# Kernel tuning notes

Hardware: AMD Instinct MI355X
Metric: run time of the kernel (lower is better)

## Reference

```python
import jax, jax.numpy as jnp
import numpy as np

N_NODES = 100000
N_EDGES = 1600000
VOCAB = 50000
F_DIM = 128
N_GRAPHS = 64
N_LABELS = 20


def setup_inputs() -> dict:
    key = jax.random.key(0)
    ks = jax.random.split(key, 12)
    s = 1.0 / np.sqrt(F_DIM)
    inp = {
        "x": jax.random.randint(ks[0], (N_NODES,), 0, VOCAB),
        "edge_index": jax.random.randint(ks[1], (2, N_EDGES), 0, N_NODES),
        "batch": jnp.sort(jax.random.randint(ks[2], (N_NODES,), 0, N_GRAPHS)),
        "emb": jax.random.normal(ks[3], (VOCAB, F_DIM), jnp.float32),
        "w1_rel": jax.random.normal(ks[4], (F_DIM, F_DIM), jnp.float32) * s,
        "w1_root": jax.random.normal(ks[5], (F_DIM, F_DIM), jnp.float32) * s,
        "b1": jnp.zeros((F_DIM,), jnp.float32),
        "w2_rel": jax.random.normal(ks[6], (F_DIM, F_DIM), jnp.float32) * s,
        "w2_root": jax.random.normal(ks[7], (F_DIM, F_DIM), jnp.float32) * s,
        "b2": jnp.zeros((F_DIM,), jnp.float32),
        "lw1": jax.random.normal(ks[8], (2 * F_DIM, 128), jnp.float32) * (1.0 / np.sqrt(2 * F_DIM)),
        "lb1": jnp.zeros((128,), jnp.float32),
        "lw2": jax.random.normal(ks[9], (128, 64), jnp.float32) * (1.0 / np.sqrt(128)),
        "lb2": jnp.zeros((64,), jnp.float32),
        "lw3": jax.random.normal(ks[10], (64, N_LABELS), jnp.float32) * (1.0 / np.sqrt(64)),
        "lb3": jnp.zeros((N_LABELS,), jnp.float32),
    }
    return inp


def graph_conv(h, src, dst, w_rel, w_root, b):
    # PyG GraphConv (aggr='add'): out_i = W_rel @ sum_{j->i} h_j + b + W_root @ h_i
    agg = jax.ops.segment_sum(h[src], dst, num_segments=N_NODES)  # [N, F]
    return agg @ w_rel + b + h @ w_root


def reference(x, edge_index, batch, emb, w1_rel, w1_root, b1,
              w2_rel, w2_root, b2, lw1, lb1, lw2, lb2, lw3, lb3):
    src, dst = edge_index[0], edge_index[1]
    h = emb[x]                                              # [N, F]
    h = jax.nn.relu(graph_conv(h, src, dst, w1_rel, w1_root, b1))
    h = jax.nn.relu(graph_conv(h, src, dst, w2_rel, w2_root, b2))
    # global max pool + global mean pool per graph
    gmax = jax.ops.segment_max(h, batch, num_segments=N_GRAPHS)  # [G, F]
    gsum = jax.ops.segment_sum(h, batch, num_segments=N_GRAPHS)
    counts = jax.ops.segment_sum(jnp.ones((N_NODES,), h.dtype), batch,
                                 num_segments=N_GRAPHS)
    gmean = gsum / jnp.maximum(counts, 1.0)[:, None]
    g = jnp.concatenate([gmax, gmean], axis=1)              # [G, 2F]
    g = jax.nn.relu(g @ lw1 + lb1)
    g = jax.nn.relu(g @ lw2 + lb2)
    # NOTE: original applies log_softmax over dim=0 (the graph dim) - kept faithful
    return jax.nn.log_softmax(g @ lw3 + lb3, axis=0)
```

## Files before the change

kernel.cpp:

```cpp
#include <hip/hip_runtime.h>
#include <hip/hip_bf16.h>

#define N_NODES   100000
#define N_EDGES   1600000
#define N_GRAPHS  64
#define FDIM      128
#define N_LABELS  20
#define NBK       64
#define P_BKT     1563
#define NCHUNKS   512
#define NCHUNKS_LOG 9
#define CHUNK     3125
#define SCAN_M    (P_BKT * NCHUNKS)
#define SB1_BLOCKS 3126
#define SB_BLOCKS 391
#define BPITCH    136

typedef __bf16 bf16x8 __attribute__((ext_vector_type(8)));
typedef float  f32x4  __attribute__((ext_vector_type(4)));
union frag_u { uint4 u; bf16x8 b; };

__device__ __forceinline__ unsigned bfr(float v) {
  unsigned b = __float_as_uint(v);
  return (b + 0x7fffu + ((b >> 16) & 1u)) >> 16;
}

__global__ __launch_bounds__(256) void prep_kernel(
    const float* __restrict__ emb, unsigned short* __restrict__ embbf,
    const float* __restrict__ w1rel, const float* __restrict__ w1rt,
    const float* __restrict__ w2rel, const float* __restrict__ w2rt,
    unsigned short* __restrict__ wt1, unsigned short* __restrict__ wt2,
    const int* __restrict__ batch, int* __restrict__ start,
    float* __restrict__ pool, float* __restrict__ zrow,
    int* __restrict__ csr, int* __restrict__ csr2,
    int* __restrict__ offsets) {
  int b = blockIdx.x;
  int tid = threadIdx.x;
  if (b < 6250) {
    int i = b * 256 + tid;
    float4 v = ((const float4*)emb)[i];
    uint2 o;
    o.x = bfr(v.x) | (bfr(v.y) << 16);
    o.y = bfr(v.z) | (bfr(v.w) << 16);
    ((uint2*)embbf)[i] = o;
  } else if (b < 6506) {
    int gid = (b - 6250) * 256 + tid;
    int l = gid >> 15;
    int rem = gid & 32767;
    int c = rem >> 8, k = rem & 255;
    const float* w = l ? ((k < 128) ? w2rel : w2rt) : ((k < 128) ? w1rel : w1rt);
    float v = w[(size_t)(k & 127) * FDIM + c];
    (l ? wt2 : wt1)[c * 256 + k] = (unsigned short)bfr(v);
  } else if (b < 6897) {
    int i = (b - 6506) * 256 + tid;
    if (i >= N_NODES) return;
    int bb = batch[i];
    int bp = (i == 0) ? -1 : batch[i - 1];
    for (int g = bp + 1; g <= bb; ++g) start[g] = i;
    if (i == N_NODES - 1) {
      for (int g = bb + 1; g <= N_GRAPHS; ++g) start[g] = N_NODES;
    }
  } else {
    int i = (b - 6897) * 256 + tid;
    if (i < N_GRAPHS * 256) pool[i] = 0.f;
    if (i < FDIM) zrow[i] = 0.f;
    if (i < 32) { csr[N_EDGES + i] = 0; csr2[N_EDGES + i] = 0; }
    if (i == 32) offsets[N_NODES] = N_EDGES;
  }
}

__global__ __launch_bounds__(256) void histA_kernel(
    const int* __restrict__ ei, int* __restrict__ cntmat) {
  __shared__ int hist[P_BKT];
  int tid = threadIdx.x;
  for (int i = tid; i < P_BKT; i += 256) hist[i] = 0;
  __syncthreads();
  int base = blockIdx.x * CHUNK;
  for (int i = tid; i < CHUNK; i += 256) {
    int d = ei[N_EDGES + base + i];
    atomicAdd(&hist[d >> 6], 1);
  }
  __syncthreads();
  for (int p = tid; p < P_BKT; p += 256)
    cntmat[p * NCHUNKS + blockIdx.x] = hist[p];
}

__global__ __launch_bounds__(256) void scanB1_kernel(
    const int* __restrict__ v, int* __restrict__ part,
    int* __restrict__ bsum) {
  __shared__ int s[256];
  int tid = threadIdx.x;
  int i = blockIdx.x * 256 + tid;
  int val = (i < SCAN_M) ? v[i] : 0;
  s[tid] = val;
  __syncthreads();
  for (int off = 1; off < 256; off <<= 1) {
    int t = (tid >= off) ? s[tid - off] : 0;
    __syncthreads();
    s[tid] += t;
    __syncthreads();
  }
  if (i < SCAN_M) part[i] = s[tid] - val;
  if (tid == 255) bsum[blockIdx.x] = s[255];
}

__global__ __launch_bounds__(512) void scanB2_kernel(int* __restrict__ bsum) {
  __shared__ int s[512];
  int tid = threadIdx.x;
  int v[8];
  int tot = 0;
#pragma unroll
  for (int j = 0; j < 8; ++j) {
    int idx = tid * 8 + j;
    v[j] = (idx < SB1_BLOCKS) ? bsum[idx] : 0;
    tot += v[j];
  }
  s[tid] = tot;
  __syncthreads();
  for (int off = 1; off < 512; off <<= 1) {
    int t = (tid >= off) ? s[tid - off] : 0;
    __syncthreads();
    s[tid] += t;
    __syncthreads();
  }
  int run = s[tid] - tot;
#pragma unroll
  for (int j = 0; j < 8; ++j) {
    int idx = tid * 8 + j;
    int val = v[j];
    if (idx < SB1_BLOCKS) bsum[idx] = run;
    run += val;
  }
}

__global__ __launch_bounds__(256) void scanB3_kernel(
    int* __restrict__ part, const int* __restrict__ bsum,
    int* __restrict__ bstart) {
  int i = blockIdx.x * 256 + threadIdx.x;
  if (i < SCAN_M) {
    int o = part[i] + bsum[blockIdx.x];
    part[i] = o;
    if ((i & (NCHUNKS - 1)) == 0) bstart[i >> NCHUNKS_LOG] = o;
  }
  if (blockIdx.x == 0 && threadIdx.x == 0) bstart[P_BKT] = N_EDGES;
}

__global__ __launch_bounds__(256) void scatA_kernel(
    const int* __restrict__ ei, const int* __restrict__ S,
    int* __restrict__ ebuf) {
  __shared__ int rc[P_BKT];
  int tid = threadIdx.x;
  for (int p = tid; p < P_BKT; p += 256)
    rc[p] = S[p * NCHUNKS + blockIdx.x];
  __syncthreads();
  int base = blockIdx.x * CHUNK;
  for (int i = tid; i < CHUNK; i += 256) {
    int s0 = ei[base + i];
    int d0 = ei[N_EDGES + base + i];
    int pos = atomicAdd(&rc[d0 >> 6], 1);
    ebuf[pos] = (s0 << 6) | (d0 & 63);
  }
}

__global__ __launch_bounds__(256) void fill2_kernel(
    const int* __restrict__ ebuf, const int* __restrict__ bstart,
    const int* __restrict__ x, int* __restrict__ offsets,
    int* __restrict__ csr, int* __restrict__ csr2) {
  __shared__ int ldeg[NBK], loffs[NBK], rc2[NBK];
  int tid = threadIdx.x;
  int p = blockIdx.x;
  int beg = bstart[p], end = bstart[p + 1];
  if (tid < NBK) ldeg[tid] = 0;
  __syncthreads();
  for (int i = beg + tid; i < end; i += 256)
    atomicAdd(&ldeg[ebuf[i] & 63], 1);
  __syncthreads();
  if (tid == 0) {
    int run = 0;
    for (int r = 0; r < NBK; ++r) { loffs[r] = run; run += ldeg[r]; }
  }
  __syncthreads();
  if (tid < NBK) {
    rc2[tid] = loffs[tid];
    int gn = p * NBK + tid;
    if (gn < N_NODES) offsets[gn] = beg + loffs[tid];
  }
  __syncthreads();
  for (int i = beg + tid; i < end; i += 256) {
    int e = ebuf[i];
    int ld = e & 63;
    int src = e >> 6;
    int pos = atomicAdd(&rc2[ld], 1);
    csr[beg + pos] = src;
    csr2[beg + pos] = x[src];
  }
}

__global__ __launch_bounds__(256) void agg_kernel(
    const unsigned short* __restrict__ feat, const int* __restrict__ srcidx,
    const int* __restrict__ offs, const float* __restrict__ zrow,
    unsigned short* __restrict__ aggout) {
  int sub = threadIdx.x >> 4;
  int fq  = threadIdx.x & 15;
  int node = blockIdx.x * 16 + sub;

  float4 e0 = make_float4(0.f, 0.f, 0.f, 0.f);
  float4 e1 = make_float4(0.f, 0.f, 0.f, 0.f);
  float4 o0 = make_float4(0.f, 0.f, 0.f, 0.f);
  float4 o1 = make_float4(0.f, 0.f, 0.f, 0.f);
  int s = offs[node], e = offs[node + 1];

  const uint4* __restrict__ fb = (const uint4*)feat;
  const uint4* __restrict__ zb = (const uint4*)zrow;

  int p = s;
  for (; p + 8 <= e; p += 8) {
    const uint4* rp[8];
#pragma unroll
    for (int u = 0; u < 8; ++u)
      rp[u] = fb + (size_t)srcidx[p + u] * 16;
    uint4 w[8];
#pragma unroll
    for (int u = 0; u < 8; ++u) w[u] = rp[u][fq];
#pragma unroll
    for (int u = 0; u < 8; ++u) {
      float4& A = (u & 1) ? o0 : e0;
      float4& B = (u & 1) ? o1 : e1;
      A.x += __uint_as_float(w[u].x << 16);
      A.y += __uint_as_float(w[u].x & 0xffff0000u);
      A.z += __uint_as_float(w[u].y << 16);
      A.w += __uint_as_float(w[u].y & 0xffff0000u);
      B.x += __uint_as_float(w[u].z << 16);
      B.y += __uint_as_float(w[u].z & 0xffff0000u);
      B.z += __uint_as_float(w[u].w << 16);
      B.w += __uint_as_float(w[u].w & 0xffff0000u);
    }
  }
  if (p < e) {
    const uint4* rp[8];
#pragma unroll
    for (int u = 0; u < 8; ++u) {
      int iu = srcidx[p + u];
      rp[u] = (p + u < e) ? (fb + (size_t)iu * 16) : zb;
    }
    uint4 w[8];
#pragma unroll
    for (int u = 0; u < 8; ++u) w[u] = rp[u][fq];
#pragma unroll
    for (int u = 0; u < 8; ++u) {
      float4& A = (u & 1) ? o0 : e0;
      float4& B = (u & 1) ? o1 : e1;
      A.x += __uint_as_float(w[u].x << 16);
      A.y += __uint_as_float(w[u].x & 0xffff0000u);
      A.z += __uint_as_float(w[u].y << 16);
      A.w += __uint_as_float(w[u].y & 0xffff0000u);
      B.x += __uint_as_float(w[u].z << 16);
      B.y += __uint_as_float(w[u].z & 0xffff0000u);
      B.z += __uint_as_float(w[u].w << 16);
      B.w += __uint_as_float(w[u].w & 0xffff0000u);
    }
  }
  float f0 = e0.x + o0.x, f1 = e0.y + o0.y, f2 = e0.z + o0.z, f3 = e0.w + o0.w;
  float f4 = e1.x + o1.x, f5 = e1.y + o1.y, f6 = e1.z + o1.z, f7 = e1.w + o1.w;
  uint4 o;
  o.x = bfr(f0) | (bfr(f1) << 16);
  o.y = bfr(f2) | (bfr(f3) << 16);
  o.z = bfr(f4) | (bfr(f5) << 16);
  o.w = bfr(f6) | (bfr(f7) << 16);
  ((uint4*)aggout)[(size_t)node * 16 + fq] = o;
}

__global__ __launch_bounds__(256, 2) void gemm_kernel(
    const unsigned short* __restrict__ aggbf,
    const unsigned short* __restrict__ rootbf,
    const int* __restrict__ hidx,
    const unsigned short* __restrict__ wt,
    const float* __restrict__ bias,
    const int* __restrict__ batch,
    float* __restrict__ pool,
    unsigned short* __restrict__ hout_bf) {
  __shared__ unsigned short B_s[128 * BPITCH];
  int tid = threadIdx.x;
  int nodeBase = blockIdx.x * 128;
  int lane = tid & 63;
  int wv = tid >> 6;
  int wbase = wv * 32;
  int lo = lane & 15, hi = lane >> 4;

  int gnode[2], hroot[2];
#pragma unroll
  for (int mt = 0; mt < 2; ++mt) {
    int g = nodeBase + wbase + mt * 16 + lo;
    if (g > N_NODES - 1) g = N_NODES - 1;
    gnode[mt] = g;
    hroot[mt] = hidx ? hidx[g] : g;
  }

  frag_u afr[2][8];
#pragma unroll
  for (int mt = 0; mt < 2; ++mt) {
#pragma unroll
    for (int t = 0; t < 4; ++t)
      afr[mt][t].u =
          *(const uint4*)(aggbf + (size_t)gnode[mt] * FDIM + t * 32 + hi * 8);
#pragma unroll
    for (int t = 0; t < 4; ++t)
      afr[mt][4 + t].u =
          *(const uint4*)(rootbf + (size_t)hroot[mt] * FDIM + t * 32 + hi * 8);
  }

  f32x4 acc[2][8];
#pragma unroll
  for (int nt = 0; nt < 8; ++nt) {
    float b = bias[nt * 16 + lo];
#pragma unroll
    for (int mt = 0; mt < 2; ++mt) {
      acc[mt][nt][0] = b; acc[mt][nt][1] = b;
      acc[mt][nt][2] = b; acc[mt][nt][3] = b;
    }
  }

  int sr = tid >> 1;
  int so = (tid & 1) * 64;

#pragma unroll
  for (int h = 0; h < 2; ++h) {
    __syncthreads();
#pragma unroll
    for (int i = 0; i < 8; ++i)
      *(uint4*)(B_s + sr * BPITCH + so + i * 8) =
          *(const uint4*)(wt + sr * 256 + h * 128 + so + i * 8);
    __syncthreads();
#pragma unroll
    for (int tt = 0; tt < 4; ++tt) {
      frag_u bfv[8];
#pragma unroll
      for (int nt = 0; nt < 8; ++nt)
        bfv[nt].u =
            *(const uint4*)&B_s[(nt * 16 + lo) * BPITCH + tt * 32 + hi * 8];
#pragma unroll
      for (int mt = 0; mt < 2; ++mt)
#pragma unroll
        for (int nt = 0; nt < 8; ++nt)
          acc[mt][nt] = __builtin_amdgcn_mfma_f32_16x16x32_bf16(
              afr[mt][h * 4 + tt].b, bfv[nt].b, acc[mt][nt], 0, 0, 0);
    }
  }

  if (hout_bf) {
#pragma unroll
    for (int mt = 0; mt < 2; ++mt) {
#pragma unroll
      for (int r = 0; r < 4; ++r) {
        int n = nodeBase + wbase + mt * 16 + hi * 4 + r;
        if (n < N_NODES) {
          unsigned short* o = hout_bf + (size_t)n * FDIM + lo;
#pragma unroll
          for (int nt = 0; nt < 8; ++nt)
            o[nt * 16] = (unsigned short)bfr(fmaxf(acc[mt][nt][r], 0.f));
        }
      }
    }
  } else {
#pragma unroll
    for (int mt = 0; mt < 2; ++mt)
#pragma unroll
      for (int nt = 0; nt < 8; ++nt)
#pragma unroll
        for (int r = 0; r < 4; ++r)
          acc[mt][nt][r] = fmaxf(acc[mt][nt][r], 0.f);

#pragma unroll
    for (int mt = 0; mt < 2; ++mt) {
      int rowBase = nodeBase + wbase + mt * 16;
      int lastRow = rowBase + 15;
      int gF = batch[rowBase < N_NODES ? rowBase : N_NODES - 1];
      int gL = batch[lastRow < N_NODES ? lastRow : N_NODES - 1];
      if (gF == gL && lastRow < N_NODES) {
#pragma unroll
        for (int nt = 0; nt < 8; ++nt) {
          float mx = fmaxf(fmaxf(acc[mt][nt][0], acc[mt][nt][1]),
                           fmaxf(acc[mt][nt][2], acc[mt][nt][3]));
          float sm = acc[mt][nt][0] + acc[mt][nt][1] +
                     acc[mt][nt][2] + acc[mt][nt][3];
          mx = fmaxf(mx, __shfl_xor(mx, 16));
          sm += __shfl_xor(sm, 16);
          mx = fmaxf(mx, __shfl_xor(mx, 32));
          sm += __shfl_xor(sm, 32);
          if (hi == 0) {
            int c = nt * 16 + lo;
            atomicMax((unsigned int*)&pool[gF * 256 + c], __float_as_uint(mx));
            atomicAdd(&pool[gF * 256 + 128 + c], sm);
          }
        }
      } else {
#pragma unroll
        for (int r = 0; r < 4; ++r) {
          int n = rowBase + hi * 4 + r;
          if (n < N_NODES) {
            int g = batch[n];
#pragma unroll
            for (int nt = 0; nt < 8; ++nt) {
              int c = nt * 16 + lo;
              atomicMax((unsigned int*)&pool[g * 256 + c],
                        __float_as_uint(acc[mt][nt][r]));
              atomicAdd(&pool[g * 256 + 128 + c], acc[mt][nt][r]);
            }
          }
        }
      }
    }
  }
}

__global__ void pool_fin_kernel(float* __restrict__ pool,
                                const int* __restrict__ start) {
  int gid = blockIdx.x * 256 + threadIdx.x;
  int g = gid >> 7, f = gid & 127;
  int cnt = start[g + 1] - start[g];
  float c = (float)(cnt > 1 ? cnt : 1);
  pool[g * 256 + 128 + f] /= c;
}

__global__ void head1_kernel(const float* __restrict__ pool,
                             const float* __restrict__ lw1,
                             const float* __restrict__ lb1,
                             float* __restrict__ t1) {
  int gid = blockIdx.x * 256 + threadIdx.x;
  int r = gid >> 7, c = gid & 127;
  float acc = lb1[c];
  for (int k = 0; k < 256; ++k) acc += pool[r * 256 + k] * lw1[k * 128 + c];
  t1[gid] = fmaxf(acc, 0.f);
}

__global__ void head2_kernel(const float* __restrict__ t1,
                             const float* __restrict__ lw2,
                             const float* __restrict__ lb2,
                             float* __restrict__ t2) {
  int gid = blockIdx.x * 256 + threadIdx.x;
  int r = gid >> 6, c = gid & 63;
  float acc = lb2[c];
  for (int k = 0; k < 128; ++k) acc += t1[r * 128 + k] * lw2[k * 64 + c];
  t2[gid] = fmaxf(acc, 0.f);
}

__global__ __launch_bounds__(256) void head3_kernel(
    const float* __restrict__ t2, const float* __restrict__ lw3,
    const float* __restrict__ lb3, float* __restrict__ out) {
  __shared__ float lg[N_GRAPHS * N_LABELS];
  __shared__ float col[N_LABELS];
  int tid = threadIdx.x;
  for (int o = tid; o < N_GRAPHS * N_LABELS; o += 256) {
    int r = o / N_LABELS, c = o - r * N_LABELS;
    float acc = lb3[c];
    for (int k = 0; k < 64; ++k) acc += t2[r * 64 + k] * lw3[k * N_LABELS + c];
    lg[o] = acc;
  }
  __syncthreads();
  if (tid < N_LABELS) {
    float m = -1e30f;
    for (int r = 0; r < N_GRAPHS; ++r) m = fmaxf(m, lg[r * N_LABELS + tid]);
    float s = 0.f;
    for (int r = 0; r < N_GRAPHS; ++r) s += expf(lg[r * N_LABELS + tid] - m);
    col[tid] = m + logf(s);
  }
  __syncthreads();
  for (int o = tid; o < N_GRAPHS * N_LABELS; o += 256) {
    int c = o % N_LABELS;
    out[o] = lg[o] - col[c];
  }
}

extern "C" void kernel_launch(void* const* d_in, const int* in_sizes, int n_in,
                              void* d_out, int out_size, void* d_ws, size_t ws_size,
                              hipStream_t stream) {
  const int*   x     = (const int*)  d_in[0];
  const int*   ei    = (const int*)  d_in[1];
  const int*   batch = (const int*)  d_in[2];
  const float* emb   = (const float*)d_in[3];
  const float* w1rel = (const float*)d_in[4];
  const float* w1rt  = (const float*)d_in[5];
  const float* b1    = (const float*)d_in[6];
  const float* w2rel = (const float*)d_in[7];
  const float* w2rt  = (const float*)d_in[8];
  const float* b2    = (const float*)d_in[9];
  const float* lw1   = (const float*)d_in[10];
  const float* lb1   = (const float*)d_in[11];
  const float* lw2   = (const float*)d_in[12];
  const float* lb2   = (const float*)d_in[13];
  const float* lw3   = (const float*)d_in[14];
  const float* lb3   = (const float*)d_in[15];
  float* out = (float*)d_out;

  char* ws = (char*)d_ws;
  const size_t HB   = 51200000;
  const size_t CSRB = 6400128;
  const size_t OFFB = 400128;
  unsigned short* embbf = (unsigned short*)(ws);
  int*   cntmat  = (int*)  (ws + 13000000);
  int*   S       = (int*)  (ws + 16500000);
  int*   bsum    = (int*)  (ws + 20000000);
  unsigned short* aggbf = (unsigned short*)(ws + HB);
  int*   ebuf    = (int*)  (ws + HB);
  int*   csr     = (int*)  (ws + 2 * HB);
  int*   csr2    = (int*)  (ws + 2 * HB + CSRB);
  int*   offsets = (int*)  (ws + 2 * HB + 2 * CSRB);
  int*   bstart  = (int*)  (ws + 2 * HB + 2 * CSRB + OFFB);
  float* zrow    = (float*)(ws + 2 * HB + 2 * CSRB + OFFB + 6400);
  int*   start   = (int*)  (ws + 2 * HB + 2 * CSRB + OFFB + 6912);
  float* pool    = (float*)(ws + 2 * HB + 2 * CSRB + OFFB + 7424);
  float* t1      = (float*)(ws + 2 * HB + 2 * CSRB + OFFB + 72960);
  float* t2      = (float*)(ws + 2 * HB + 2 * CSRB + OFFB + 105728);
  unsigned short* hbf =
      (unsigned short*)(ws + 2 * HB + 2 * CSRB + OFFB + 122112);
  unsigned short* wt1 =
      (unsigned short*)(ws + 2 * HB + 2 * CSRB + OFFB + 122112 + 25600000);
  unsigned short* wt2 = wt1 + 128 * 256;

  prep_kernel<<<6961, 256, 0, stream>>>(emb, embbf, w1rel, w1rt, w2rel, w2rt,
                                        wt1, wt2, batch, start, pool, zrow,
                                        csr, csr2, offsets);

  histA_kernel<<<NCHUNKS, 256, 0, stream>>>(ei, cntmat);
  scanB1_kernel<<<SB1_BLOCKS, 256, 0, stream>>>(cntmat, S, bsum);
  scanB2_kernel<<<1, 512, 0, stream>>>(bsum);
  scanB3_kernel<<<SB1_BLOCKS, 256, 0, stream>>>(S, bsum, bstart);
  scatA_kernel<<<NCHUNKS, 256, 0, stream>>>(ei, S, ebuf);
  fill2_kernel<<<P_BKT, 256, 0, stream>>>(ebuf, bstart, x, offsets, csr, csr2);

  agg_kernel<<<N_NODES / 16, 256, 0, stream>>>(embbf, csr2, offsets, zrow, aggbf);
  gemm_kernel<<<(N_NODES + 127) / 128, 256, 0, stream>>>(
      aggbf, embbf, x, wt1, b1, (const int*)nullptr, (float*)nullptr, hbf);

  agg_kernel<<<N_NODES / 16, 256, 0, stream>>>(hbf, csr, offsets, zrow, aggbf);
  gemm_kernel<<<(N_NODES + 127) / 128, 256, 0, stream>>>(
      aggbf, hbf, (const int*)nullptr, wt2, b2, batch, pool,
      (unsigned short*)nullptr);

  pool_fin_kernel<<<32, 256, 0, stream>>>(pool, start);

  head1_kernel<<<32, 256, 0, stream>>>(pool, lw1, lb1, t1);
  head2_kernel<<<16, 256, 0, stream>>>(t1, lw2, lb2, t2);
  head3_kernel<<<1, 256, 0, stream>>>(t2, lw3, lb3, out);
}
```

Measured before the change: 370.9 us.

## Replace per-chunk count matrix scan with global bucket atomics and fuse head kernels

```diff
diff --git a/kernel.cpp b/kernel.cpp
--- a/kernel.cpp
+++ b/kernel.cpp
@@ -9,10 +9,7 @@
 #define NBK       64
 #define P_BKT     1563
 #define NCHUNKS   512
-#define NCHUNKS_LOG 9
 #define CHUNK     3125
-#define SCAN_M    (P_BKT * NCHUNKS)
-#define SB1_BLOCKS 3126
 #define SB_BLOCKS 391
 #define BPITCH    136
 
@@ -33,7 +30,7 @@
     const int* __restrict__ batch, int* __restrict__ start,
     float* __restrict__ pool, float* __restrict__ zrow,
     int* __restrict__ csr, int* __restrict__ csr2,
-    int* __restrict__ offsets) {
+    int* __restrict__ offsets, int* __restrict__ btot) {
   int b = blockIdx.x;
   int tid = threadIdx.x;
   if (b < 6250) {
@@ -63,14 +60,15 @@
   } else {
     int i = (b - 6897) * 256 + tid;
     if (i < N_GRAPHS * 256) pool[i] = 0.f;
+    if (i < P_BKT) btot[i] = 0;
     if (i < FDIM) zrow[i] = 0.f;
     if (i < 32) { csr[N_EDGES + i] = 0; csr2[N_EDGES + i] = 0; }
     if (i == 32) offsets[N_NODES] = N_EDGES;
   }
 }
 
-__global__ __launch_bounds__(256) void histA_kernel(
-    const int* __restrict__ ei, int* __restrict__ cntmat) {
+__global__ __launch_bounds__(256) void histB_kernel(
+    const int* __restrict__ ei, int* __restrict__ btot) {
   __shared__ int hist[P_BKT];
   int tid = threadIdx.x;
   for (int i = tid; i < P_BKT; i += 256) hist[i] = 0;
@@ -81,38 +79,23 @@
     atomicAdd(&hist[d >> 6], 1);
   }
   __syncthreads();
-  for (int p = tid; p < P_BKT; p += 256)
-    cntmat[p * NCHUNKS + blockIdx.x] = hist[p];
-}
-
-__global__ __launch_bounds__(256) void scanB1_kernel(
-    const int* __restrict__ v, int* __restrict__ part,
-    int* __restrict__ bsum) {
-  __shared__ int s[256];
-  int tid = threadIdx.x;
-  int i = blockIdx.x * 256 + tid;
-  int val = (i < SCAN_M) ? v[i] : 0;
-  s[tid] = val;
-  __syncthreads();
-  for (int off = 1; off < 256; off <<= 1) {
-    int t = (tid >= off) ? s[tid - off] : 0;
-    __syncthreads();
-    s[tid] += t;
-    __syncthreads();
-  }
-  if (i < SCAN_M) part[i] = s[tid] - val;
-  if (tid == 255) bsum[blockIdx.x] = s[255];
-}
-
-__global__ __launch_bounds__(512) void scanB2_kernel(int* __restrict__ bsum) {
+  for (int p = tid; p < P_BKT; p += 256) {
+    int c = hist[p];
+    if (c) atomicAdd(&btot[p], c);
+  }
+}
+
+__global__ __launch_bounds__(512) void scanBkt_kernel(
+    const int* __restrict__ btot, int* __restrict__ bstart,
+    int* __restrict__ gcur) {
   __shared__ int s[512];
   int tid = threadIdx.x;
-  int v[8];
+  int v[4];
   int tot = 0;
 #pragma unroll
-  for (int j = 0; j < 8; ++j) {
-    int idx = tid * 8 + j;
-    v[j] = (idx < SB1_BLOCKS) ? bsum[idx] : 0;
+  for (int j = 0; j < 4; ++j) {
+    int idx = tid * 4 + j;
+    v[j] = (idx < P_BKT) ? btot[idx] : 0;
     tot += v[j];
   }
   s[tid] = tot;
@@ -125,35 +108,32 @@
   }
   int run = s[tid] - tot;
 #pragma unroll
-  for (int j = 0; j < 8; ++j) {
-    int idx = tid * 8 + j;
-    int val = v[j];
-    if (idx < SB1_BLOCKS) bsum[idx] = run;
-    run += val;
-  }
-}
-
-__global__ __launch_bounds__(256) void scanB3_kernel(
-    int* __restrict__ part, const int* __restrict__ bsum,
-    int* __restrict__ bstart) {
-  int i = blockIdx.x * 256 + threadIdx.x;
-  if (i < SCAN_M) {
-    int o = part[i] + bsum[blockIdx.x];
-    part[i] = o;
-    if ((i & (NCHUNKS - 1)) == 0) bstart[i >> NCHUNKS_LOG] = o;
-  }
-  if (blockIdx.x == 0 && threadIdx.x == 0) bstart[P_BKT] = N_EDGES;
-}
-
-__global__ __launch_bounds__(256) void scatA_kernel(
-    const int* __restrict__ ei, const int* __restrict__ S,
+  for (int j = 0; j < 4; ++j) {
+    int idx = tid * 4 + j;
+    if (idx < P_BKT) { bstart[idx] = run; gcur[idx] = run; }
+    run += v[j];
+  }
+  if (tid == 0) bstart[P_BKT] = N_EDGES;
+}
+
+__global__ __launch_bounds__(256) void scatB_kernel(
+    const int* __restrict__ ei, int* __restrict__ gcur,
     int* __restrict__ ebuf) {
   __shared__ int rc[P_BKT];
   int tid = threadIdx.x;
-  for (int p = tid; p < P_BKT; p += 256)
-    rc[p] = S[p * NCHUNKS + blockIdx.x];
+  for (int p = tid; p < P_BKT; p += 256) rc[p] = 0;
   __syncthreads();
   int base = blockIdx.x * CHUNK;
+  for (int i = tid; i < CHUNK; i += 256) {
+    int d = ei[N_EDGES + base + i];
+    atomicAdd(&rc[d >> 6], 1);
+  }
+  __syncthreads();
+  for (int p = tid; p < P_BKT; p += 256) {
+    int c = rc[p];
+    rc[p] = c ? atomicAdd(&gcur[p], c) : 0;
+  }
+  __syncthreads();
   for (int i = tid; i < CHUNK; i += 256) {
     int s0 = ei[base + i];
     int d0 = ei[N_EDGES + base + i];
@@ -413,47 +393,42 @@
   }
 }
 
-__global__ void pool_fin_kernel(float* __restrict__ pool,
-                                const int* __restrict__ start) {
-  int gid = blockIdx.x * 256 + threadIdx.x;
-  int g = gid >> 7, f = gid & 127;
-  int cnt = start[g + 1] - start[g];
-  float c = (float)(cnt > 1 ? cnt : 1);
-  pool[g * 256 + 128 + f] /= c;
-}
-
 __global__ void head1_kernel(const float* __restrict__ pool,
+                             const int* __restrict__ start,
                              const float* __restrict__ lw1,
                              const float* __restrict__ lb1,
                              float* __restrict__ t1) {
   int gid = blockIdx.x * 256 + threadIdx.x;
   int r = gid >> 7, c = gid & 127;
-  float acc = lb1[c];
-  for (int k = 0; k < 256; ++k) acc += pool[r * 256 + k] * lw1[k * 128 + c];
-  t1[gid] = fmaxf(acc, 0.f);
-}
-
-__global__ void head2_kernel(const float* __restrict__ t1,
-                             const float* __restrict__ lw2,
-                             const float* __restrict__ lb2,
-                             float* __restrict__ t2) {
-  int gid = blockIdx.x * 256 + threadIdx.x;
-  int r = gid >> 6, c = gid & 63;
-  float acc = lb2[c];
-  for (int k = 0; k < 128; ++k) acc += t1[r * 128 + k] * lw2[k * 64 + c];
-  t2[gid] = fmaxf(acc, 0.f);
-}
-
-__global__ __launch_bounds__(256) void head3_kernel(
-    const float* __restrict__ t2, const float* __restrict__ lw3,
-    const float* __restrict__ lb3, float* __restrict__ out) {
+  int cnt = start[r + 1] - start[r];
+  float inv = 1.f / (float)(cnt > 1 ? cnt : 1);
+  float a0 = 0.f, a1 = 0.f;
+  for (int k = 0; k < 128; ++k) a0 += pool[r * 256 + k] * lw1[k * 128 + c];
+  for (int k = 0; k < 128; ++k)
+    a1 += pool[r * 256 + 128 + k] * lw1[(128 + k) * 128 + c];
+  t1[gid] = fmaxf(lb1[c] + a0 + a1 * inv, 0.f);
+}
+
+__global__ __launch_bounds__(256) void head23_kernel(
+    const float* __restrict__ t1,
+    const float* __restrict__ lw2, const float* __restrict__ lb2,
+    const float* __restrict__ lw3, const float* __restrict__ lb3,
+    float* __restrict__ out) {
+  __shared__ float t2s[N_GRAPHS * 64];
   __shared__ float lg[N_GRAPHS * N_LABELS];
   __shared__ float col[N_LABELS];
   int tid = threadIdx.x;
+  for (int o = tid; o < N_GRAPHS * 64; o += 256) {
+    int r = o >> 6, c = o & 63;
+    float acc = lb2[c];
+    for (int k = 0; k < 128; ++k) acc += t1[r * 128 + k] * lw2[k * 64 + c];
+    t2s[o] = fmaxf(acc, 0.f);
+  }
+  __syncthreads();
   for (int o = tid; o < N_GRAPHS * N_LABELS; o += 256) {
     int r = o / N_LABELS, c = o - r * N_LABELS;
     float acc = lb3[c];
-    for (int k = 0; k < 64; ++k) acc += t2[r * 64 + k] * lw3[k * N_LABELS + c];
+    for (int k = 0; k < 64; ++k) acc += t2s[r * 64 + k] * lw3[k * N_LABELS + c];
     lg[o] = acc;
   }
   __syncthreads();
@@ -497,9 +472,8 @@
   const size_t CSRB = 6400128;
   const size_t OFFB = 400128;
   unsigned short* embbf = (unsigned short*)(ws);
-  int*   cntmat  = (int*)  (ws + 13000000);
-  int*   S       = (int*)  (ws + 16500000);
-  int*   bsum    = (int*)  (ws + 20000000);
+  int*   btot    = (int*)  (ws + 13000000);
+  int*   gcur    = (int*)  (ws + 13100000);
   unsigned short* aggbf = (unsigned short*)(ws + HB);
   int*   ebuf    = (int*)  (ws + HB);
   int*   csr     = (int*)  (ws + 2 * HB);
@@ -510,7 +484,6 @@
   int*   start   = (int*)  (ws + 2 * HB + 2 * CSRB + OFFB + 6912);
   float* pool    = (float*)(ws + 2 * HB + 2 * CSRB + OFFB + 7424);
   float* t1      = (float*)(ws + 2 * HB + 2 * CSRB + OFFB + 72960);
-  float* t2      = (float*)(ws + 2 * HB + 2 * CSRB + OFFB + 105728);
   unsigned short* hbf =
       (unsigned short*)(ws + 2 * HB + 2 * CSRB + OFFB + 122112);
   unsigned short* wt1 =
@@ -519,13 +492,11 @@
 
   prep_kernel<<<6961, 256, 0, stream>>>(emb, embbf, w1rel, w1rt, w2rel, w2rt,
                                         wt1, wt2, batch, start, pool, zrow,
-                                        csr, csr2, offsets);
-
-  histA_kernel<<<NCHUNKS, 256, 0, stream>>>(ei, cntmat);
-  scanB1_kernel<<<SB1_BLOCKS, 256, 0, stream>>>(cntmat, S, bsum);
-  scanB2_kernel<<<1, 512, 0, stream>>>(bsum);
-  scanB3_kernel<<<SB1_BLOCKS, 256, 0, stream>>>(S, bsum, bstart);
-  scatA_kernel<<<NCHUNKS, 256, 0, stream>>>(ei, S, ebuf);
+                                        csr, csr2, offsets, btot);
+
+  histB_kernel<<<NCHUNKS, 256, 0, stream>>>(ei, btot);
+  scanBkt_kernel<<<1, 512, 0, stream>>>(btot, bstart, gcur);
+  scatB_kernel<<<NCHUNKS, 256, 0, stream>>>(ei, gcur, ebuf);
   fill2_kernel<<<P_BKT, 256, 0, stream>>>(ebuf, bstart, x, offsets, csr, csr2);
 
   agg_kernel<<<N_NODES / 16, 256, 0, stream>>>(embbf, csr2, offsets, zrow, aggbf);
@@ -537,9 +508,6 @@
       aggbf, hbf, (const int*)nullptr, wt2, b2, batch, pool,
       (unsigned short*)nullptr);
 
-  pool_fin_kernel<<<32, 256, 0, stream>>>(pool, start);
-
-  head1_kernel<<<32, 256, 0, stream>>>(pool, lw1, lb1, t1);
-  head2_kernel<<<16, 256, 0, stream>>>(t1, lw2, lb2, t2);
-  head3_kernel<<<1, 256, 0, stream>>>(t2, lw3, lb3, out);
-}
+  head1_kernel<<<32, 256, 0, stream>>>(pool, start, lw1, lb1, t1);
+  head23_kernel<<<1, 256, 0, stream>>>(t1, lw2, lb2, lw3, lb3, out);
+}
```

After: 428.5 us. +15.5%, slower.
